# Performance work log

Hardware: AMD Instinct MI355X
Metric: run time of the kernel (lower is better)

The kernel has to match this reference:

```python
import jax, jax.numpy as jnp
from jax import lax
import numpy as np

EPS = 1e-3  # keras BatchNormalization default epsilon

def _bn(x, g, b, m, v):
    return (x - m) / jnp.sqrt(v + EPS) * g + b

def _conv_relu(x, w, b):
    y = lax.conv_general_dilated(x, w, (1, 1), 'SAME', dimension_numbers=('NHWC', 'HWIO', 'NHWC'))
    return jax.nn.relu(y + b)

def _pool(x):
    return lax.reduce_window(x, -jnp.inf, lax.max, (1, 2, 2, 1), (1, 2, 2, 1), 'VALID')

def setup_inputs():
    key = jax.random.key(0)
    ks = jax.random.split(key, 24)
    B, E = 2048, 16
    rn = lambda k, s, sc=0.05: jax.random.normal(k, s, jnp.float32) * sc
    pos = lambda k, s: jax.random.uniform(k, s, jnp.float32, 0.5, 1.5)
    inp = {}
    inp['x'] = jax.random.normal(ks[0], (B, 32, 32, 3), jnp.float32)
    inp['cW1'] = rn(ks[1], (3, 3, 3, 32), 0.2); inp['cb1'] = jnp.zeros((32,), jnp.float32)
    inp['bn1g'] = pos(ks[2], (32,)); inp['bn1b'] = rn(ks[3], (32,))
    inp['bn1m'] = rn(ks[4], (32,)); inp['bn1v'] = pos(ks[5], (32,))
    inp['cW2'] = rn(ks[6], (3, 3, 32, 64), 0.1); inp['cb2'] = jnp.zeros((64,), jnp.float32)
    inp['bn2g'] = pos(ks[7], (64,)); inp['bn2b'] = rn(ks[8], (64,))
    inp['bn2m'] = rn(ks[9], (64,)); inp['bn2v'] = pos(ks[10], (64,))
    inp['dW'] = rn(ks[11], (4096, 128), 0.02); inp['db'] = jnp.zeros((128,), jnp.float32)
    inp['rW1'] = rn(ks[12], (128, 64), 0.1); inp['rb1'] = jnp.zeros((64,), jnp.float32)
    inp['rW2'] = rn(ks[13], (64, E), 0.1); inp['rb2'] = jnp.zeros((E,), jnp.float32)
    inp['eW1'] = rn(ks[14], (E, 128, 128), 0.1); inp['eb1'] = jnp.zeros((E, 128), jnp.float32)
    inp['ebng'] = pos(ks[15], (E, 128)); inp['ebnb'] = rn(ks[16], (E, 128))
    inp['ebnm'] = rn(ks[17], (E, 128)); inp['ebnv'] = pos(ks[18], (E, 128))
    inp['eW2'] = rn(ks[19], (E, 128, 64), 0.1); inp['eb2'] = jnp.zeros((E, 64), jnp.float32)
    inp['eW3'] = rn(ks[20], (E, 64, 10), 0.1); inp['eb3'] = jnp.zeros((E, 10), jnp.float32)
    return inp

def reference(x, cW1, cb1, bn1g, bn1b, bn1m, bn1v, cW2, cb2, bn2g, bn2b, bn2m, bn2v,
              dW, db, rW1, rb1, rW2, rb2, eW1, eb1, ebng, ebnb, ebnm, ebnv, eW2, eb2, eW3, eb3):
    # shared trunk: conv(relu) -> BN -> maxpool, twice; flatten; dense(relu). Dropout = identity (inference).
    h = _pool(_bn(_conv_relu(x, cW1, cb1), bn1g, bn1b, bn1m, bn1v))   # [B,16,16,32]
    h = _pool(_bn(_conv_relu(h, cW2, cb2), bn2g, bn2b, bn2m, bn2v))   # [B,8,8,64]
    feats = jax.nn.relu(h.reshape(h.shape[0], -1) @ dW + db)          # [B,128]
    # router softmax over expert logits
    router_logits = jax.nn.relu(feats @ rW1 + rb1) @ rW2 + rb2        # [B,E]
    router_probs = jax.nn.softmax(router_logits, axis=-1)
    # all experts fused into batched GEMMs over stacked weights: [E,B,*]
    e = jax.nn.relu(jnp.einsum('bd,edh->ebh', feats, eW1) + eb1[:, None, :])
    e = _bn(e, ebng[:, None, :], ebnb[:, None, :], ebnm[:, None, :], ebnv[:, None, :])
    e = jax.nn.relu(jnp.einsum('ebh,ehk->ebk', e, eW2) + eb2[:, None, :])
    e = jnp.einsum('ebk,ekc->ebc', e, eW3) + eb3[:, None, :]          # [E,B,10]
    # weighted sum combine: sum_e probs[b,e] * logits[e,b,c]
    return jnp.einsum('ebc,be->bc', e, router_probs)
```

## Files before the change

kernel.cpp:

```cpp
#include <hip/hip_runtime.h>

#define EPS 1e-3f

typedef _Float16 half8 __attribute__((ext_vector_type(8)));
typedef _Float16 half4v __attribute__((ext_vector_type(4)));
typedef float f32x4 __attribute__((ext_vector_type(4)));

__global__ __launch_bounds__(256) void k_wprep_all(
    const float* __restrict__ dW,  _Float16* __restrict__ Wt2,
    const float* __restrict__ eW1, _Float16* __restrict__ eW1t,
    const float* __restrict__ eW2, _Float16* __restrict__ eW2t,
    const float* __restrict__ cW1, _Float16* __restrict__ Wt1,
    const float* __restrict__ cW2, _Float16* __restrict__ Wt,
    const float* __restrict__ eW3, _Float16* __restrict__ eW3p)
{
    __shared__ _Float16 lsbuf[16640];
    int bx = blockIdx.x, tid = threadIdx.x;

    if (bx < 64) {
        auto lt = (_Float16(*)[137])lsbuf;
        int kb = bx * 64;
        int c = tid & 127, r2 = tid >> 7;
#pragma unroll
        for (int it = 0; it < 32; ++it) {
            int r = it * 2 + r2;
            lt[r][c] = (_Float16)dW[(long)(kb + r) * 128 + c];
        }
        __syncthreads();
#pragma unroll
        for (int it = 0; it < 4; ++it) {
            int chunk = it * 256 + tid;
            int n = chunk >> 3, kc = (chunk & 7) * 8;
            half8 v;
#pragma unroll
            for (int j = 0; j < 8; ++j) v[j] = lt[kc + j][n];
            *(half8*)(Wt2 + (long)n * 4096 + kb + kc) = v;
        }
    } else if (bx < 80) {
        auto lt = (_Float16(*)[130])lsbuf;
        int e = bx - 64;
        const float* src = eW1 + (long)e * 16384;
#pragma unroll
        for (int it = 0; it < 64; ++it) {
            int idx = it * 256 + tid;
            lt[idx >> 7][idx & 127] = (_Float16)src[idx];
        }
        __syncthreads();
        _Float16* dst = eW1t + (long)e * 16384;
#pragma unroll
        for (int it = 0; it < 64; ++it) {
            int idx = it * 256 + tid;
            dst[idx] = lt[idx & 127][idx >> 7];
        }
    } else if (bx < 96) {
        auto lt = (_Float16(*)[66])lsbuf;
        int e = bx - 80;
        const float* src = eW2 + (long)e * 8192;
#pragma unroll
        for (int it = 0; it < 32; ++it) {
            int idx = it * 256 + tid;
            lt[idx >> 6][idx & 63] = (_Float16)src[idx];
        }
        __syncthreads();
        _Float16* dst = eW2t + (long)e * 8192;
#pragma unroll
        for (int it = 0; it < 32; ++it) {
            int idx = it * 256 + tid;
            dst[idx] = lt[idx & 127][idx >> 7];
        }
    } else {
        int t = (bx - 96) * 256 + tid;
        if (t < 2048) {
            int k = t & 31, co = (t >> 5) & 31, p = t >> 10;
            int kyin = (k >> 4) & 1, kxp = (k >> 2) & 3, ci = k & 3;
            int ky = 2 * p + kyin;
            float val = (ky < 3 && kxp < 3 && ci < 3)
                        ? cW1[((ky * 3 + kxp) * 3 + ci) * 32 + co] : 0.f;
            Wt1[t] = (_Float16)val;
        } else if (t >= 3072 && t < 3072 + 18432) {
            int u = t - 3072;
            int co = u & 63;
            int rest = u >> 6;
            int ci = rest & 31, tap = rest >> 5;
            Wt[(tap * 64 + co) * 32 + ci] = (_Float16)cW2[u];
        } else if (t >= 21504 && t < 21504 + 16384) {
            int u = t - 21504;
            int k = u & 63, n = (u >> 6) & 15, e = u >> 10;
            float val = (n < 10) ? eW3[(e * 64 + k) * 10 + n] : 0.f;
            eW3p[(e * 16 + n) * 64 + k] = (_Float16)val;
        }
    }
}

__global__ __launch_bounds__(256) void k_conv12(
    const float* __restrict__ x, const _Float16* __restrict__ Wt1,
    const float* __restrict__ b1, const float* __restrict__ g1,
    const float* __restrict__ bb1, const float* __restrict__ m1,
    const float* __restrict__ v1,
    const _Float16* __restrict__ Wt,
    const float* __restrict__ b2, const float* __restrict__ g2,
    const float* __restrict__ bb2, const float* __restrict__ m2,
    const float* __restrict__ v2,
    _Float16* __restrict__ out)
{
    __shared__ __align__(16) _Float16 As1[35][40][4];
    __shared__ __align__(16) _Float16 As2[18][18][40];
    int tid = threadIdx.x;
    int b = blockIdx.x;
    int w = tid >> 6, l = tid & 63;
    int l15 = l & 15, lq = l >> 4;
    int lqr = lq >> 1, lqc = (lq & 1) * 2;

    {
        float4 z = make_float4(0.f, 0.f, 0.f, 0.f);
        float4* f1p = (float4*)&As1[0][0][0];
        for (int i = tid; i < 700; i += 256) f1p[i] = z;
        float4* f2p = (float4*)&As2[0][0][0];
        for (int i = tid; i < 1620; i += 256) f2p[i] = z;
    }
    __syncthreads();

    {
        int y = tid >> 3, x0 = (tid & 7) * 4;
        const float* src = x + ((long)b * 1024 + y * 32 + x0) * 3;
        float4 f0 = *(const float4*)(src);
        float4 f1 = *(const float4*)(src + 4);
        float4 f2 = *(const float4*)(src + 8);
        half4v h0 = { (_Float16)f0.x, (_Float16)f0.y, (_Float16)f0.z, (_Float16)0.f };
        half4v h1 = { (_Float16)f0.w, (_Float16)f1.x, (_Float16)f1.y, (_Float16)0.f };
        half4v h2 = { (_Float16)f1.z, (_Float16)f1.w, (_Float16)f2.x, (_Float16)0.f };
        half4v h3 = { (_Float16)f2.y, (_Float16)f2.z, (_Float16)f2.w, (_Float16)0.f };
        *(half4v*)&As1[y + 1][x0 + 1][0] = h0;
        *(half4v*)&As1[y + 1][x0 + 2][0] = h1;
        *(half4v*)&As1[y + 1][x0 + 3][0] = h2;
        *(half4v*)&As1[y + 1][x0 + 4][0] = h3;
    }

    half8 bf1[2][2];
#pragma unroll
    for (int p = 0; p < 2; ++p)
#pragma unroll
        for (int nf = 0; nf < 2; ++nf)
            bf1[p][nf] = *(const half8*)(Wt1 + (p * 32 + nf * 16 + l15) * 32 + lq * 8);

    float bv1[2], S1[2], T1[2];
#pragma unroll
    for (int nf = 0; nf < 2; ++nf) {
        int co = nf * 16 + l15;
        bv1[nf] = b1[co];
        float s = rsqrtf(v1[co] + EPS) * g1[co];
        S1[nf] = s;
        T1[nf] = bb1[co] - m1[co] * s;
    }
    __syncthreads();

    {
        int y0 = w * 8;
#pragma unroll
        for (int pr = 0; pr < 4; ++pr) {
            int ya = y0 + 2 * pr;
            f32x4 acc[2][2][2];
#pragma unroll
            for (int r = 0; r < 2; ++r)
#pragma unroll
                for (int h = 0; h < 2; ++h)
#pragma unroll
                    for (int nf = 0; nf < 2; ++nf)
                        acc[r][h][nf] = (f32x4){ bv1[nf], bv1[nf], bv1[nf], bv1[nf] };

#pragma unroll
            for (int p = 0; p < 2; ++p)
#pragma unroll
                for (int r = 0; r < 2; ++r)
#pragma unroll
                    for (int h = 0; h < 2; ++h) {
                        const _Float16* ap = &As1[ya + r + 2 * p + lqr][h * 16 + l15 + lqc][0];
                        half4v a0 = *(const half4v*)ap;
                        half4v a1 = *(const half4v*)(ap + 4);
                        half8 af = __builtin_shufflevector(a0, a1, 0, 1, 2, 3, 4, 5, 6, 7);
#pragma unroll
                        for (int nf = 0; nf < 2; ++nf)
                            acc[r][h][nf] = __builtin_amdgcn_mfma_f32_16x16x32_f16(
                                af, bf1[p][nf], acc[r][h][nf], 0, 0, 0);
                    }

            int py = w * 4 + pr;
#pragma unroll
            for (int h = 0; h < 2; ++h)
#pragma unroll
                for (int nf = 0; nf < 2; ++nf) {
                    f32x4 aA = acc[0][h][nf], aB = acc[1][h][nf];
                    float p0 = fmaxf(fmaxf(aA[0], aA[1]), fmaxf(aB[0], aB[1]));
                    float p1 = fmaxf(fmaxf(aA[2], aA[3]), fmaxf(aB[2], aB[3]));
                    p0 = fmaxf(p0, 0.f); p1 = fmaxf(p1, 0.f);
                    p0 = fmaf(p0, S1[nf], T1[nf]);
                    p1 = fmaf(p1, S1[nf], T1[nf]);
                    int px = h * 8 + lq * 2;
                    int co = nf * 16 + l15;
                    As2[py + 1][px + 1][co] = (_Float16)p0;
                    As2[py + 1][px + 2][co] = (_Float16)p1;
                }
        }
    }
    __syncthreads();

    f32x4 acc2[4][4];
#pragma unroll
    for (int nf = 0; nf < 4; ++nf) {
        float bv = b2[nf * 16 + l15];
#pragma unroll
        for (int mf = 0; mf < 4; ++mf)
            acc2[mf][nf] = (f32x4){ bv, bv, bv, bv };
    }

    int row0 = 4 * w;
#pragma unroll
    for (int tap = 0; tap < 9; ++tap) {
        int ky = tap / 3, kx = tap % 3;
        half8 bf[4];
        const _Float16* wb = Wt + ((long)(tap * 64 + l15)) * 32 + lq * 8;
#pragma unroll
        for (int nf = 0; nf < 4; ++nf)
            bf[nf] = *(const half8*)(wb + (long)nf * 16 * 32);
#pragma unroll
        for (int mf = 0; mf < 4; ++mf) {
            const _Float16* ap = &As2[row0 + mf + ky][l15 + kx][lq * 8];
            half8 af = *(const half8*)ap;
#pragma unroll
            for (int nf = 0; nf < 4; ++nf)
                acc2[mf][nf] = __builtin_amdgcn_mfma_f32_16x16x32_f16(
                    af, bf[nf], acc2[mf][nf], 0, 0, 0);
        }
    }

#pragma unroll
    for (int nf = 0; nf < 4; ++nf) {
        int co = nf * 16 + l15;
        float s = rsqrtf(v2[co] + EPS) * g2[co];
        float t2 = bb2[co] - m2[co] * s;
#pragma unroll
        for (int pr = 0; pr < 2; ++pr) {
            int prow = 2 * w + pr;
            f32x4 a0 = acc2[2 * pr][nf];
            f32x4 a1 = acc2[2 * pr + 1][nf];
            float p0 = fmaxf(fmaxf(a0[0], a0[1]), fmaxf(a1[0], a1[1]));
            float p1 = fmaxf(fmaxf(a0[2], a0[3]), fmaxf(a1[2], a1[3]));
            p0 = fmaxf(p0, 0.f);
            p1 = fmaxf(p1, 0.f);
            int ppx = lq * 2;
            long base = (((long)b * 8 + prow) * 8) * 64 + co;
            out[base + (long)(ppx    ) * 64] = (_Float16)fmaf(p0, s, t2);
            out[base + (long)(ppx + 1) * 64] = (_Float16)fmaf(p1, s, t2);
        }
    }
}

__global__ __launch_bounds__(256) void k_dense_mfma(
    const _Float16* __restrict__ h2f, const _Float16* __restrict__ Wt2,
    float* __restrict__ pws)
{
    __shared__ __align__(16) _Float16 As[16][264];
    int tid = threadIdx.x;
    int w = tid >> 6, l = tid & 63;
    int l15 = l & 15, lq = l >> 4;
    int brow = blockIdx.x * 16;
    int kbase = blockIdx.y * 512;
    int n0 = w * 32;

    f32x4 acc[2] = { (f32x4){0.f,0.f,0.f,0.f}, (f32x4){0.f,0.f,0.f,0.f} };

    int srow = tid >> 4, sc = (tid & 15) * 16;
#pragma unroll
    for (int k0 = 0; k0 < 512; k0 += 256) {
        __syncthreads();
        const _Float16* src = h2f + (long)(brow + srow) * 4096 + kbase + k0 + sc;
        half8 v0 = *(const half8*)src;
        half8 v1 = *(const half8*)(src + 8);
        *(half8*)(&As[srow][sc])     = v0;
        *(half8*)(&As[srow][sc + 8]) = v1;
        __syncthreads();
#pragma unroll
        for (int kk = 0; kk < 256; kk += 32) {
            half8 af = *(const half8*)(&As[l15][kk + lq * 8]);
#pragma unroll
            for (int nf = 0; nf < 2; ++nf) {
                half8 bf = *(const half8*)(Wt2 + (long)(n0 + nf * 16 + l15) * 4096
                                           + kbase + k0 + kk + lq * 8);
                acc[nf] = __builtin_amdgcn_mfma_f32_16x16x32_f16(af, bf, acc[nf], 0, 0, 0);
            }
        }
    }

    float* pbase = pws + (long)blockIdx.y * 262144;
#pragma unroll
    for (int nf = 0; nf < 2; ++nf) {
        int n = n0 + nf * 16 + l15;
#pragma unroll
        for (int reg = 0; reg < 4; ++reg) {
            int b = brow + lq * 4 + reg;
            pbase[(long)b * 128 + n] = acc[nf][reg];
        }
    }
}

__global__ __launch_bounds__(256) void k_reduce_router(
    const float* __restrict__ pws, const float* __restrict__ db,
    const float* __restrict__ rW1, const float* __restrict__ rb1,
    const float* __restrict__ rW2, const float* __restrict__ rb2,
    _Float16* __restrict__ featsH, float* __restrict__ probs)
{
    __shared__ float fsm[8][128];
    __shared__ float r1s[8][64];
    int tid = threadIdx.x;
    int brow = blockIdx.x * 8;
    int r = tid >> 5, c0 = (tid & 31) * 4;

    float acc[4];
#pragma unroll
    for (int j = 0; j < 4; ++j) acc[j] = db[c0 + j];
    long base = (long)(brow + r) * 128 + c0;
#pragma unroll
    for (int kc = 0; kc < 8; ++kc) {
        float4 v0 = *(const float4*)(pws + (long)kc * 262144 + base);
        acc[0] += v0.x; acc[1] += v0.y; acc[2] += v0.z; acc[3] += v0.w;
    }
    half4v hv;
#pragma unroll
    for (int j = 0; j < 4; ++j) {
        float val = fmaxf(acc[j], 0.f);
        fsm[r][c0 + j] = val;
        hv[j] = (_Float16)val;
    }
    *(half4v*)(featsH + base) = hv;
    __syncthreads();

    {
        int h = tid & 63, bg = tid >> 6;
        float a[2];
#pragma unroll
        for (int i = 0; i < 2; ++i) a[i] = rb1[h];
        for (int d = 0; d < 128; ++d) {
            float wgt = rW1[d * 64 + h];
#pragma unroll
            for (int i = 0; i < 2; ++i) a[i] += fsm[bg * 2 + i][d] * wgt;
        }
#pragma unroll
        for (int i = 0; i < 2; ++i) r1s[bg * 2 + i][h] = fmaxf(a[i], 0.f);
    }
    __syncthreads();

    if (tid < 128) {
        int b = tid >> 4, e = tid & 15;
        float a = rb2[e];
#pragma unroll 8
        for (int k = 0; k < 64; ++k) a += r1s[b][k] * rW2[k * 16 + e];
        float mx = a;
#pragma unroll
        for (int off = 1; off < 16; off <<= 1)
            mx = fmaxf(mx, __shfl_xor(mx, off, 16));
        float ex = __expf(a - mx);
        float s = ex;
#pragma unroll
        for (int off = 1; off < 16; off <<= 1)
            s += __shfl_xor(s, off, 16);
        probs[(long)(brow + b) * 16 + e] = ex / s;
    }
}

__global__ __launch_bounds__(512) void k_expert_mfma(
    const _Float16* __restrict__ featsH,
    const _Float16* __restrict__ eW1t, const float* __restrict__ eb1,
    const float* __restrict__ g,  const float* __restrict__ bb,
    const float* __restrict__ m,  const float* __restrict__ v,
    const _Float16* __restrict__ eW2t, const float* __restrict__ eb2,
    const _Float16* __restrict__ eW3p, const float* __restrict__ eb3,
    float* __restrict__ e3p)
{
    __shared__ __align__(16) _Float16 fsH[64][136];
    __shared__ __align__(16) _Float16 h1sH[64][136];
    __shared__ __align__(16) _Float16 h2sH[64][72];
    int e = blockIdx.x, bt = blockIdx.y;
    int tid = threadIdx.x;
    int w = tid >> 6, l = tid & 63, l15 = l & 15, lq = l >> 4;
    int brow = bt * 64;
    int m0 = (w & 3) * 16;
    int nh = w >> 2;

#pragma unroll
    for (int it = 0; it < 2; ++it) {
        int idx = it * 512 + tid;
        int r = idx >> 4, c = (idx & 15) * 8;
        *(half8*)&fsH[r][c] = *(const half8*)(featsH + (long)(brow + r) * 128 + c);
    }
    __syncthreads();

    {
        half8 af[4];
#pragma unroll
        for (int kq = 0; kq < 4; ++kq)
            af[kq] = *(const half8*)&fsH[m0 + l15][kq * 32 + lq * 8];
        const _Float16* B1 = eW1t + (long)e * 16384 + (long)nh * 8192 + l15 * 128 + lq * 8;
        f32x4 acc[4];
#pragma unroll
        for (int nf = 0; nf < 4; ++nf) {
            float bv = eb1[e * 128 + nh * 64 + nf * 16 + l15];
            acc[nf] = (f32x4){ bv, bv, bv, bv };
        }
#pragma unroll
        for (int nf = 0; nf < 4; ++nf)
#pragma unroll
            for (int kq = 0; kq < 4; ++kq) {
                half8 bfv = *(const half8*)(B1 + nf * 2048 + kq * 32);
                acc[nf] = __builtin_amdgcn_mfma_f32_16x16x32_f16(af[kq], bfv, acc[nf], 0, 0, 0);
            }
#pragma unroll
        for (int nf = 0; nf < 4; ++nf) {
            int h = nh * 64 + nf * 16 + l15;
            float gg = g[e * 128 + h], bbv = bb[e * 128 + h], mm = m[e * 128 + h];
            float iv = rsqrtf(v[e * 128 + h] + EPS);
#pragma unroll
            for (int reg = 0; reg < 4; ++reg) {
                float val = fmaxf(acc[nf][reg], 0.f);
                h1sH[m0 + lq * 4 + reg][h] = (_Float16)((val - mm) * iv * gg + bbv);
            }
        }
    }
    __syncthreads();

    {
        half8 af[4];
#pragma unroll
        for (int kq = 0; kq < 4; ++kq)
            af[kq] = *(const half8*)&h1sH[m0 + l15][kq * 32 + lq * 8];
        const _Float16* B2 = eW2t + (long)e * 8192 + (long)nh * 4096 + l15 * 128 + lq * 8;
        f32x4 acc[2];
#pragma unroll
        for (int nf = 0; nf < 2; ++nf) {
            float bv = eb2[e * 64 + nh * 32 + nf * 16 + l15];
            acc[nf] = (f32x4){ bv, bv, bv, bv };
        }
#pragma unroll
        for (int nf = 0; nf < 2; ++nf)
#pragma unroll
            for (int kq = 0; kq < 4; ++kq) {
                half8 bfv = *(const half8*)(B2 + nf * 2048 + kq * 32);
                acc[nf] = __builtin_amdgcn_mfma_f32_16x16x32_f16(af[kq], bfv, acc[nf], 0, 0, 0);
            }
#pragma unroll
        for (int nf = 0; nf < 2; ++nf)
#pragma unroll
            for (int reg = 0; reg < 4; ++reg)
                h2sH[m0 + lq * 4 + reg][nh * 32 + nf * 16 + l15] =
                    (_Float16)fmaxf(acc[nf][reg], 0.f);
    }
    __syncthreads();

    if (nh == 0) {
        half8 af[2];
#pragma unroll
        for (int kq = 0; kq < 2; ++kq)
            af[kq] = *(const half8*)&h2sH[m0 + l15][kq * 32 + lq * 8];
        const _Float16* B3 = eW3p + (long)e * 1024 + l15 * 64 + lq * 8;
        float bv = (l15 < 10) ? eb3[e * 10 + l15] : 0.f;
        f32x4 acc = (f32x4){ bv, bv, bv, bv };
#pragma unroll
        for (int kq = 0; kq < 2; ++kq) {
            half8 bfv = *(const half8*)(B3 + kq * 32);
            acc = __builtin_amdgcn_mfma_f32_16x16x32_f16(af[kq], bfv, acc, 0, 0, 0);
        }
#pragma unroll
        for (int reg = 0; reg < 4; ++reg) {
            int b = brow + m0 + lq * 4 + reg;
            e3p[((long)e * 2048 + b) * 16 + l15] = acc[reg];
        }
    }
}

__global__ __launch_bounds__(256) void k_combine(
    const float* __restrict__ e3p, const float* __restrict__ probs,
    float* __restrict__ out)
{
    int t = blockIdx.x * blockDim.x + threadIdx.x;
    if (t >= 2048 * 10) return;
    int b = t / 10, c = t % 10;
    float acc = 0.f;
#pragma unroll
    for (int e = 0; e < 16; ++e)
        acc += probs[(long)b * 16 + e] * e3p[((long)e * 2048 + b) * 16 + c];
    out[t] = acc;
}

extern "C" void kernel_launch(void* const* d_in, const int* in_sizes, int n_in,
                              void* d_out, int out_size, void* d_ws, size_t ws_size,
                              hipStream_t stream)
{
    const float* x    = (const float*)d_in[0];
    const float* cW1  = (const float*)d_in[1];
    const float* cb1  = (const float*)d_in[2];
    const float* bn1g = (const float*)d_in[3];
    const float* bn1b = (const float*)d_in[4];
    const float* bn1m = (const float*)d_in[5];
    const float* bn1v = (const float*)d_in[6];
    const float* cW2  = (const float*)d_in[7];
    const float* cb2  = (const float*)d_in[8];
    const float* bn2g = (const float*)d_in[9];
    const float* bn2b = (const float*)d_in[10];
    const float* bn2m = (const float*)d_in[11];
    const float* bn2v = (const float*)d_in[12];
    const float* dW   = (const float*)d_in[13];
    const float* db   = (const float*)d_in[14];
    const float* rW1  = (const float*)d_in[15];
    const float* rb1  = (const float*)d_in[16];
    const float* rW2  = (const float*)d_in[17];
    const float* rb2  = (const float*)d_in[18];
    const float* eW1  = (const float*)d_in[19];
    const float* eb1  = (const float*)d_in[20];
    const float* ebng = (const float*)d_in[21];
    const float* ebnb = (const float*)d_in[22];
    const float* ebnm = (const float*)d_in[23];
    const float* ebnv = (const float*)d_in[24];
    const float* eW2  = (const float*)d_in[25];
    const float* eb2  = (const float*)d_in[26];
    const float* eW3  = (const float*)d_in[27];
    const float* eb3  = (const float*)d_in[28];

    float* ws    = (float*)d_ws;
    float* h1reg = ws;
    float* e3p   = h1reg;
    _Float16* featsH = (_Float16*)(h1reg + 524288);
    float* h2reg = h1reg + 16777216;
    _Float16* h2f = (_Float16*)h2reg;
    _Float16* Wt2 = (_Float16*)(h2reg + 4194304);
    float* probs = h2reg + 8388608;
    float* ewreg = probs + 32768;
    _Float16* eW1t = (_Float16*)ewreg;
    _Float16* eW2t = eW1t + 262144;
    _Float16* eW3p = eW2t + 131072;
    _Float16* Wt   = eW3p + 16384;
    _Float16* Wt1  = Wt + 18432;
    float* pws   = ewreg + 262144;
    float* out   = (float*)d_out;

    k_wprep_all<<<244, 256, 0, stream>>>(dW, Wt2, eW1, eW1t, eW2, eW2t,
                                         cW1, Wt1, cW2, Wt, eW3, eW3p);
    k_conv12<<<2048, 256, 0, stream>>>(x, Wt1, cb1, bn1g, bn1b, bn1m, bn1v,
                                       Wt, cb2, bn2g, bn2b, bn2m, bn2v, h2f);
    {
        dim3 grid(128, 8);
        k_dense_mfma<<<grid, 256, 0, stream>>>(h2f, Wt2, pws);
    }
    k_reduce_router<<<256, 256, 0, stream>>>(pws, db, rW1, rb1, rW2, rb2,
                                             featsH, probs);
    {
        dim3 grid(16, 32);
        k_expert_mfma<<<grid, 512, 0, stream>>>(featsH, eW1t, eb1, ebng, ebnb, ebnm, ebnv,
                                                eW2t, eb2, eW3p, eb3, e3p);
    }
    k_combine<<<80, 256, 0, stream>>>(e3p, probs, out);
}
```

Before: 87.75 us.

## Split fused conv kernel into two row-halves per image with halo recompute

The fused conv1+conv2 kernel now launches two blocks per image, each covering half of the output rows. Each block loads a 20-row input slab and recomputes one halo row of pooled conv1 output for conv2. This roughly halves shared memory per block and doubles the grid, aiming for higher occupancy and better latency hiding. The cost is redundant halo compute, uneven conv1 work across warps (warp 0 does three pooled rows), and a scalar, less coalesced input load.

```diff
diff --git a/kernel.cpp b/kernel.cpp
--- a/kernel.cpp
+++ b/kernel.cpp
@@ -103,37 +103,34 @@
     const float* __restrict__ v2,
     _Float16* __restrict__ out)
 {
-    __shared__ __align__(16) _Float16 As1[35][40][4];
-    __shared__ __align__(16) _Float16 As2[18][18][40];
+    __shared__ __align__(16) _Float16 As1[21][36][4];
+    __shared__ __align__(16) _Float16 As2[10][18][40];
     int tid = threadIdx.x;
-    int b = blockIdx.x;
+    int b  = blockIdx.x;
+    int hh = blockIdx.y;
     int w = tid >> 6, l = tid & 63;
     int l15 = l & 15, lq = l >> 4;
     int lqr = lq >> 1, lqc = (lq & 1) * 2;
+    int start  = 7 * hh;
+    int gstart = 14 * hh - 1;
 
     {
         float4 z = make_float4(0.f, 0.f, 0.f, 0.f);
         float4* f1p = (float4*)&As1[0][0][0];
-        for (int i = tid; i < 700; i += 256) f1p[i] = z;
+        for (int i = tid; i < 378; i += 256) f1p[i] = z;
         float4* f2p = (float4*)&As2[0][0][0];
-        for (int i = tid; i < 1620; i += 256) f2p[i] = z;
-    }
-    __syncthreads();
-
-    {
-        int y = tid >> 3, x0 = (tid & 7) * 4;
-        const float* src = x + ((long)b * 1024 + y * 32 + x0) * 3;
-        float4 f0 = *(const float4*)(src);
-        float4 f1 = *(const float4*)(src + 4);
-        float4 f2 = *(const float4*)(src + 8);
-        half4v h0 = { (_Float16)f0.x, (_Float16)f0.y, (_Float16)f0.z, (_Float16)0.f };
-        half4v h1 = { (_Float16)f0.w, (_Float16)f1.x, (_Float16)f1.y, (_Float16)0.f };
-        half4v h2 = { (_Float16)f1.z, (_Float16)f1.w, (_Float16)f2.x, (_Float16)0.f };
-        half4v h3 = { (_Float16)f2.y, (_Float16)f2.z, (_Float16)f2.w, (_Float16)0.f };
-        *(half4v*)&As1[y + 1][x0 + 1][0] = h0;
-        *(half4v*)&As1[y + 1][x0 + 2][0] = h1;
-        *(half4v*)&As1[y + 1][x0 + 3][0] = h2;
-        *(half4v*)&As1[y + 1][x0 + 4][0] = h3;
+        for (int i = tid; i < 900; i += 256) f2p[i] = z;
+    }
+    __syncthreads();
+
+    for (int i = tid; i < 640; i += 256) {
+        int row = i >> 5, px = i & 31;
+        int g = gstart + row;
+        if ((unsigned)g < 32u) {
+            const float* src = x + ((long)b * 1024 + g * 32 + px) * 3;
+            half4v hv = { (_Float16)src[0], (_Float16)src[1], (_Float16)src[2], (_Float16)0.f };
+            *(half4v*)&As1[row][px + 1][0] = hv;
+        }
     }
 
     half8 bf1[2][2];
@@ -155,65 +152,64 @@
     __syncthreads();
 
     {
-        int y0 = w * 8;
-#pragma unroll
-        for (int pr = 0; pr < 4; ++pr) {
-            int ya = y0 + 2 * pr;
+        int qstart = (w == 0) ? 0 : (2 * w + 1);
+        int qcnt   = (w == 0) ? 3 : 2;
+        for (int qq = 0; qq < qcnt; ++qq) {
+            int q = qstart + qq;
             f32x4 acc[2][2][2];
 #pragma unroll
             for (int r = 0; r < 2; ++r)
 #pragma unroll
-                for (int h = 0; h < 2; ++h)
+                for (int xh = 0; xh < 2; ++xh)
 #pragma unroll
                     for (int nf = 0; nf < 2; ++nf)
-                        acc[r][h][nf] = (f32x4){ bv1[nf], bv1[nf], bv1[nf], bv1[nf] };
+                        acc[r][xh][nf] = (f32x4){ bv1[nf], bv1[nf], bv1[nf], bv1[nf] };
 
 #pragma unroll
             for (int p = 0; p < 2; ++p)
 #pragma unroll
                 for (int r = 0; r < 2; ++r)
 #pragma unroll
-                    for (int h = 0; h < 2; ++h) {
-                        const _Float16* ap = &As1[ya + r + 2 * p + lqr][h * 16 + l15 + lqc][0];
+                    for (int xh = 0; xh < 2; ++xh) {
+                        const _Float16* ap = &As1[2 * q + r + 2 * p + lqr][xh * 16 + l15 + lqc][0];
                         half4v a0 = *(const half4v*)ap;
                         half4v a1 = *(const half4v*)(ap + 4);
                         half8 af = __builtin_shufflevector(a0, a1, 0, 1, 2, 3, 4, 5, 6, 7);
 #pragma unroll
                         for (int nf = 0; nf < 2; ++nf)
-                            acc[r][h][nf] = __builtin_amdgcn_mfma_f32_16x16x32_f16(
-                                af, bf1[p][nf], acc[r][h][nf], 0, 0, 0);
+                            acc[r][xh][nf] = __builtin_amdgcn_mfma_f32_16x16x32_f16(
+                                af, bf1[p][nf], acc[r][xh][nf], 0, 0, 0);
                     }
 
-            int py = w * 4 + pr;
-#pragma unroll
-            for (int h = 0; h < 2; ++h)
+            int a2row = q + 1 - hh;
+#pragma unroll
+            for (int xh = 0; xh < 2; ++xh)
 #pragma unroll
                 for (int nf = 0; nf < 2; ++nf) {
-                    f32x4 aA = acc[0][h][nf], aB = acc[1][h][nf];
+                    f32x4 aA = acc[0][xh][nf], aB = acc[1][xh][nf];
                     float p0 = fmaxf(fmaxf(aA[0], aA[1]), fmaxf(aB[0], aB[1]));
                     float p1 = fmaxf(fmaxf(aA[2], aA[3]), fmaxf(aB[2], aB[3]));
                     p0 = fmaxf(p0, 0.f); p1 = fmaxf(p1, 0.f);
                     p0 = fmaf(p0, S1[nf], T1[nf]);
                     p1 = fmaf(p1, S1[nf], T1[nf]);
-                    int px = h * 8 + lq * 2;
+                    int px = xh * 8 + lq * 2;
                     int co = nf * 16 + l15;
-                    As2[py + 1][px + 1][co] = (_Float16)p0;
-                    As2[py + 1][px + 2][co] = (_Float16)p1;
+                    As2[a2row][px + 1][co] = (_Float16)p0;
+                    As2[a2row][px + 2][co] = (_Float16)p1;
                 }
         }
     }
     __syncthreads();
 
-    f32x4 acc2[4][4];
+    f32x4 acc2[2][4];
 #pragma unroll
     for (int nf = 0; nf < 4; ++nf) {
         float bv = b2[nf * 16 + l15];
 #pragma unroll
-        for (int mf = 0; mf < 4; ++mf)
+        for (int mf = 0; mf < 2; ++mf)
             acc2[mf][nf] = (f32x4){ bv, bv, bv, bv };
     }
 
-    int row0 = 4 * w;
 #pragma unroll
     for (int tap = 0; tap < 9; ++tap) {
         int ky = tap / 3, kx = tap % 3;
@@ -223,8 +219,8 @@
         for (int nf = 0; nf < 4; ++nf)
             bf[nf] = *(const half8*)(wb + (long)nf * 16 * 32);
 #pragma unroll
-        for (int mf = 0; mf < 4; ++mf) {
-            const _Float16* ap = &As2[row0 + mf + ky][l15 + kx][lq * 8];
+        for (int mf = 0; mf < 2; ++mf) {
+            const _Float16* ap = &As2[2 * w + mf + ky][l15 + kx][lq * 8];
             half8 af = *(const half8*)ap;
 #pragma unroll
             for (int nf = 0; nf < 4; ++nf)
@@ -233,16 +229,15 @@
         }
     }
 
-#pragma unroll
-    for (int nf = 0; nf < 4; ++nf) {
-        int co = nf * 16 + l15;
-        float s = rsqrtf(v2[co] + EPS) * g2[co];
-        float t2 = bb2[co] - m2[co] * s;
-#pragma unroll
-        for (int pr = 0; pr < 2; ++pr) {
-            int prow = 2 * w + pr;
-            f32x4 a0 = acc2[2 * pr][nf];
-            f32x4 a1 = acc2[2 * pr + 1][nf];
+    {
+        int prow = hh * 4 + w;
+#pragma unroll
+        for (int nf = 0; nf < 4; ++nf) {
+            int co = nf * 16 + l15;
+            float s = rsqrtf(v2[co] + EPS) * g2[co];
+            float t2 = bb2[co] - m2[co] * s;
+            f32x4 a0 = acc2[0][nf];
+            f32x4 a1 = acc2[1][nf];
             float p0 = fmaxf(fmaxf(a0[0], a0[1]), fmaxf(a1[0], a1[1]));
             float p1 = fmaxf(fmaxf(a0[2], a0[3]), fmaxf(a1[2], a1[3]));
             p0 = fmaxf(p0, 0.f);
@@ -543,8 +538,11 @@
 
     k_wprep_all<<<244, 256, 0, stream>>>(dW, Wt2, eW1, eW1t, eW2, eW2t,
                                          cW1, Wt1, cW2, Wt, eW3, eW3p);
-    k_conv12<<<2048, 256, 0, stream>>>(x, Wt1, cb1, bn1g, bn1b, bn1m, bn1v,
-                                       Wt, cb2, bn2g, bn2b, bn2m, bn2v, h2f);
+    {
+        dim3 grid(2048, 2);
+        k_conv12<<<grid, 256, 0, stream>>>(x, Wt1, cb1, bn1g, bn1b, bn1m, bn1v,
+                                           Wt, cb2, bn2g, bn2b, bn2m, bn2v, h2f);
+    }
     {
         dim3 grid(128, 8);
         k_dense_mfma<<<grid, 256, 0, stream>>>(h2f, Wt2, pws);
```

New measurement: 108.0 us. 23.1% more time.

## Zero only halo borders in conv LDS and store dense partials in fp16

Applied to the files above, without the earlier changes.

The conv kernel now zeroes only the padding border cells of its two shared-memory tiles instead of clearing both tiles entirely, and drops the barrier that followed the clear. The split-K dense kernel writes its partial sums as fp16 instead of fp32, and the reduce kernel reads them as fp16, halving that intermediate traffic. The fp16 partials lose precision in the split-K reduction. Removing the barrier relies on interior cells being fully overwritten and on later barriers ordering the border writes before they are read.

```diff
diff --git a/kernel.cpp b/kernel.cpp
--- a/kernel.cpp
+++ b/kernel.cpp
@@ -112,13 +112,24 @@
     int lqr = lq >> 1, lqc = (lq & 1) * 2;
 
     {
+        half4v z4 = { (_Float16)0.f, (_Float16)0.f, (_Float16)0.f, (_Float16)0.f };
+        for (int i = tid; i < 216; i += 256) {
+            int row, col;
+            if (i < 120) { int rr = i / 40; row = (rr == 0) ? 0 : 32 + rr; col = i % 40; }
+            else         { int j = i - 120; row = 1 + j / 3; int cc = j % 3; col = (cc == 0) ? 0 : 32 + cc; }
+            *(half4v*)&As1[row][col][0] = z4;
+        }
         float4 z = make_float4(0.f, 0.f, 0.f, 0.f);
-        float4* f1p = (float4*)&As1[0][0][0];
-        for (int i = tid; i < 700; i += 256) f1p[i] = z;
-        float4* f2p = (float4*)&As2[0][0][0];
-        for (int i = tid; i < 1620; i += 256) f2p[i] = z;
-    }
-    __syncthreads();
+        for (int i = tid; i < 272; i += 256) {
+            int pair = i >> 2, q = i & 3;
+            int row, col;
+            if      (pair < 18) { row = 0;  col = pair; }
+            else if (pair < 36) { row = 17; col = pair - 18; }
+            else if (pair < 52) { row = pair - 36 + 1; col = 0; }
+            else                { row = pair - 52 + 1; col = 17; }
+            *(float4*)&As2[row][col][q * 8] = z;
+        }
+    }
 
     {
         int y = tid >> 3, x0 = (tid & 7) * 4;
@@ -257,7 +268,7 @@
 
 __global__ __launch_bounds__(256) void k_dense_mfma(
     const _Float16* __restrict__ h2f, const _Float16* __restrict__ Wt2,
-    float* __restrict__ pws)
+    _Float16* __restrict__ pws)
 {
     __shared__ __align__(16) _Float16 As[16][264];
     int tid = threadIdx.x;
@@ -291,20 +302,20 @@
         }
     }
 
-    float* pbase = pws + (long)blockIdx.y * 262144;
+    _Float16* pbase = pws + (long)blockIdx.y * 262144;
 #pragma unroll
     for (int nf = 0; nf < 2; ++nf) {
         int n = n0 + nf * 16 + l15;
 #pragma unroll
         for (int reg = 0; reg < 4; ++reg) {
             int b = brow + lq * 4 + reg;
-            pbase[(long)b * 128 + n] = acc[nf][reg];
+            pbase[(long)b * 128 + n] = (_Float16)acc[nf][reg];
         }
     }
 }
 
 __global__ __launch_bounds__(256) void k_reduce_router(
-    const float* __restrict__ pws, const float* __restrict__ db,
+    const _Float16* __restrict__ pws, const float* __restrict__ db,
     const float* __restrict__ rW1, const float* __restrict__ rb1,
     const float* __restrict__ rW2, const float* __restrict__ rb2,
     _Float16* __restrict__ featsH, float* __restrict__ probs)
@@ -321,8 +332,9 @@
     long base = (long)(brow + r) * 128 + c0;
 #pragma unroll
     for (int kc = 0; kc < 8; ++kc) {
-        float4 v0 = *(const float4*)(pws + (long)kc * 262144 + base);
-        acc[0] += v0.x; acc[1] += v0.y; acc[2] += v0.z; acc[3] += v0.w;
+        half4v v0 = *(const half4v*)(pws + (long)kc * 262144 + base);
+#pragma unroll
+        for (int j = 0; j < 4; ++j) acc[j] += (float)v0[j];
     }
     half4v hv;
 #pragma unroll
@@ -538,7 +550,7 @@
     _Float16* eW3p = eW2t + 131072;
     _Float16* Wt   = eW3p + 16384;
     _Float16* Wt1  = Wt + 18432;
-    float* pws   = ewreg + 262144;
+    _Float16* pws = (_Float16*)(ewreg + 262144);
     float* out   = (float*)d_out;
 
     k_wprep_all<<<244, 256, 0, stream>>>(dW, Wt2, eW1, eW1t, eW2, eW2t,
```

Result: no change. 86.53 us (-1.4%).
